# Kernel optimization log

Hardware: AMD Instinct MI355X
Metric: run time of the kernel (lower is better)

Reference implementation:

```python
import jax, jax.numpy as jnp
import numpy as np

EMBED = 1024
HEADS = 16


def setup_inputs() -> dict:
    key = jax.random.key(0)
    ks = jax.random.split(key, 12)
    s = 1.0 / np.sqrt(EMBED)
    return {
        "x": jax.random.normal(ks[0], (1, EMBED, 128, 128), jnp.float32),
        "masks": jax.random.normal(ks[1], (200, 128, 128), jnp.float32),
        "Wq": jax.random.normal(ks[2], (EMBED, EMBED), jnp.float32) * s,
        "bq": jax.random.normal(ks[3], (EMBED,), jnp.float32) * 0.02,
        "Wk": jax.random.normal(ks[4], (EMBED, EMBED), jnp.float32) * s,
        "bk": jax.random.normal(ks[5], (EMBED,), jnp.float32) * 0.02,
        "Wv": jax.random.normal(ks[6], (EMBED, EMBED), jnp.float32) * s,
        "bv": jax.random.normal(ks[7], (EMBED,), jnp.float32) * 0.02,
        "Wc": jax.random.normal(ks[8], (EMBED, EMBED), jnp.float32) * s,
        "bc": jax.random.normal(ks[9], (EMBED,), jnp.float32) * 0.02,
    }


def reference(x, masks, Wq, bq, Wk, bk, Wv, bv, Wc, bc):
    # x: [1, C, H, W], masks: [Q, H, W]  (way4 branch, batch must be 1)
    N, C, H, W = x.shape
    Q = masks.shape[0]
    HW = H * W
    nh = HEADS
    hd = C // nh

    xs = x.reshape(C, HW).T                      # [HW, C] pixel tokens
    m = jax.nn.sigmoid(masks).reshape(Q, HW).T   # [HW, Q]

    # mask-weighted mean pooling (avoid materializing [HW, Q, C])
    w = jnp.sum(m, axis=0)                       # [Q]
    mean = jnp.einsum('lq,lc->qc', m, xs) / (w[:, None] + 0.001)  # [Q, C]

    seq = jnp.concatenate([mean, xs], axis=0)    # [L, C], L = Q + HW
    L = Q + HW

    q = (mean @ Wq.T + bq).reshape(Q, nh, hd) * (hd ** -0.5)
    k = (seq @ Wk.T + bk).reshape(L, nh, hd)
    v = (seq @ Wv.T + bv).reshape(L, nh, hd)

    # bool attn mask [Q, L]: True = disallowed
    qq = ~jnp.eye(Q, dtype=bool)                 # only self among pooled queries
    qp = (m.T <= 0.9)                            # pixels with sigmoid <= 0.9 masked
    attn_mask = jnp.concatenate([qq, qp], axis=1)  # [Q, L]

    scores = jnp.einsum('qhd,lhd->hql', q, k)    # [nh, Q, L]
    scores = jnp.where(attn_mask[None], -jnp.inf, scores)
    probs = jax.nn.softmax(scores, axis=-1)
    ctx = jnp.einsum('hql,lhd->qhd', probs, v).reshape(Q, C)
    out = ctx @ Wc.T + bc                        # [Q, out_dim]
    return out.reshape(Q, 1, -1)                 # match torch [Q, batch=1, out_dim]
```

## Files before the change

### kernel.cpp

```cpp
#include <hip/hip_runtime.h>
#include <math.h>

#define HW_  16384
#define Q_   200
#define C_   1024
#define L_   16584
#define NH_  16
#define HD_  64
#define CAP  512
#define KSPLIT 8
#define KCH  (HW_ / KSPLIT)
#define ASPLIT 4
#define SK   8

typedef __attribute__((ext_vector_type(8))) __bf16 bf16x8;
typedef __attribute__((ext_vector_type(8))) unsigned short u16x8;
typedef __attribute__((ext_vector_type(4))) unsigned short u16x4;
typedef __attribute__((ext_vector_type(4))) float f32x4;

__device__ inline unsigned short f2bf(float f) {
  unsigned int u = __float_as_uint(f);
  u += 0x7fff + ((u >> 16) & 1);
  return (unsigned short)(u >> 16);
}
__device__ inline float bf2f(unsigned short u) {
  return __uint_as_float((unsigned int)u << 16);
}


__global__ __launch_bounds__(256) void k_sig_compact(const float* __restrict__ masks,
                                                     unsigned short* __restrict__ msigbf,
                                                     float* __restrict__ w,
                                                     int* __restrict__ cnt,
                                                     int* __restrict__ idxg) {
  int q = blockIdx.x;
  int tid = threadIdx.x;
  unsigned short* obf = msigbf + (size_t)q * HW_;
  if (q >= Q_) {
    u16x4 z = {0, 0, 0, 0};
    for (int i = tid; i < HW_ / 4; i += 256) *(u16x4*)&obf[i * 4] = z;
    return;
  }
  const float* mrow = masks + (size_t)q * HW_;
  const int base = tid * 64;
  unsigned long long bits = 0;
  float s = 0.f;
  #pragma unroll
  for (int j4 = 0; j4 < 16; j4++) {
    float4 v = *(const float4*)&mrow[base + j4 * 4];
    float sg0 = 1.f / (1.f + expf(-v.x));
    float sg1 = 1.f / (1.f + expf(-v.y));
    float sg2 = 1.f / (1.f + expf(-v.z));
    float sg3 = 1.f / (1.f + expf(-v.w));
    u16x4 o = {f2bf(sg0), f2bf(sg1), f2bf(sg2), f2bf(sg3)};
    *(u16x4*)&obf[base + j4 * 4] = o;
    s += sg0 + sg1 + sg2 + sg3;
    if (sg0 > 0.9f) bits |= 1ull << (j4 * 4 + 0);
    if (sg1 > 0.9f) bits |= 1ull << (j4 * 4 + 1);
    if (sg2 > 0.9f) bits |= 1ull << (j4 * 4 + 2);
    if (sg3 > 0.9f) bits |= 1ull << (j4 * 4 + 3);
  }
  int my = __popcll(bits);

  __shared__ float red[256];
  __shared__ int sc[256];
  red[tid] = s;
  sc[tid] = my;
  __syncthreads();
  for (int off = 128; off > 0; off >>= 1) {
    if (tid < off) red[tid] += red[tid + off];
    __syncthreads();
  }
  if (tid == 0) w[q] = red[0];
  for (int off = 1; off < 256; off <<= 1) {
    int v = sc[tid];
    int add = (tid >= off) ? sc[tid - off] : 0;
    __syncthreads();
    sc[tid] = v + add;
    __syncthreads();
  }
  int excl = sc[tid] - my;
  int total = sc[255];
  int* orow = idxg + (size_t)q * CAP;
  int off = 1 + excl;
  for (int j = 0; j < 64; j++) {
    if ((bits >> j) & 1ull) {
      if (off < CAP) orow[off] = Q_ + base + j;
      off++;
    }
  }
  if (tid == 0) {
    orow[0] = q;
    int c = 1 + total;
    cnt[q] = c < CAP ? c : CAP;
  }
}

__global__ __launch_bounds__(256) void k_xcast(const float* __restrict__ x,
                                               unsigned short* __restrict__ xbf,
                                               unsigned short* __restrict__ seqbf) {
  __shared__ float t[32][33];
  int l0 = blockIdx.x * 32, c0 = blockIdx.y * 32;
  int tx = threadIdx.x, ty = threadIdx.y;
  #pragma unroll
  for (int i = 0; i < 32; i += 8) {
    float v = x[(size_t)(c0 + ty + i) * HW_ + l0 + tx];
    t[ty + i][tx] = v;
    xbf[(size_t)(c0 + ty + i) * HW_ + l0 + tx] = f2bf(v);
  }
  __syncthreads();
  #pragma unroll
  for (int i = 0; i < 32; i += 8)
    seqbf[(size_t)(Q_ + l0 + ty + i) * C_ + c0 + tx] = f2bf(t[tx][ty + i]);
}

__global__ __launch_bounds__(256) void k_cast4(const float* __restrict__ s0,
                                               const float* __restrict__ s1,
                                               const float* __restrict__ s2,
                                               const float* __restrict__ s3,
                                               unsigned short* __restrict__ d0,
                                               unsigned short* __restrict__ d1,
                                               unsigned short* __restrict__ d2,
                                               unsigned short* __restrict__ d3) {
  const float* src = (blockIdx.y == 0) ? s0 : (blockIdx.y == 1) ? s1
                     : (blockIdx.y == 2) ? s2 : s3;
  unsigned short* dst = (blockIdx.y == 0) ? d0 : (blockIdx.y == 1) ? d1
                        : (blockIdx.y == 2) ? d2 : d3;
  int i = (blockIdx.x * 256 + threadIdx.x) * 4;
  float4 v = *(const float4*)&src[i];
  u16x4 o = {f2bf(v.x), f2bf(v.y), f2bf(v.z), f2bf(v.w)};
  *(u16x4*)&dst[i] = o;
}

#define GBM 128
#define GBN 128
#define GBK 32

__global__ __launch_bounds__(256, 2) void k_gemm_kv(const unsigned short* __restrict__ A,
                                                    const unsigned short* __restrict__ Bk,
                                                    const unsigned short* __restrict__ Bv,
                                                    const float* __restrict__ bk,
                                                    const float* __restrict__ bv,
                                                    unsigned short* __restrict__ Ko,
                                                    unsigned short* __restrict__ Vo,
                                                    int M, int K) {
  __shared__ __attribute__((aligned(16))) unsigned short smem[3][3 * GBM * GBK];
  int w = blockIdx.x;
  int nbm = gridDim.x >> 3;
  int t = (w >> 3) + (w & 7) * nbm;
  int bm = (t >> 3) * GBM;
  int bn = (t & 7) * GBN;
  int tid = threadIdx.x;
  int wid = tid >> 6, lane = tid & 63;
  int half = wid >> 1;
  int whalf = wid & 1;
  int fq = lane >> 4, fr = lane & 15;
  int srow = lane >> 2;
  int scol = (((lane & 3) ^ ((lane >> 3) & 3)) * 8);
  int sslot = (fq ^ ((fr >> 1) & 3)) * 8;
  int boff = (half == 0) ? GBM * GBK : 2 * GBM * GBK;

  auto stage = [&](int buf, int k0) {
    #pragma unroll
    for (int i = 0; i < 6; i++) {
      int ci = wid * 6 + i;
      const unsigned short* src;
      if (ci < 8) {
        int gA = bm + ci * 16 + srow; if (gA > M - 1) gA = M - 1;
        src = A + (size_t)gA * K + k0 + scol;
      } else if (ci < 16) {
        src = Bk + (size_t)(bn + (ci - 8) * 16 + srow) * K + k0 + scol;
      } else {
        src = Bv + (size_t)(bn + (ci - 16) * 16 + srow) * K + k0 + scol;
      }
      __builtin_amdgcn_global_load_lds(
          (const __attribute__((address_space(1))) void*)src,
          (__attribute__((address_space(3))) void*)((char*)&smem[buf][0] + ci * 1024),
          16, 0, 0);
    }
  };

  f32x4 acc[4][8] = {};
  const int NT = K / GBK;
  stage(0, 0);
  stage(1, GBK);
  for (int it = 0; it < NT; it++) {
    int cur = it % 3;
    if (it + 2 < NT) {
      stage((it + 2) % 3, (it + 2) * GBK);
      asm volatile("s_waitcnt vmcnt(12)" ::: "memory");
    } else if (it + 1 < NT) {
      asm volatile("s_waitcnt vmcnt(6)" ::: "memory");
    } else {
      asm volatile("s_waitcnt vmcnt(0)" ::: "memory");
    }
    __builtin_amdgcn_s_barrier();
    asm volatile("" ::: "memory");
    const unsigned short (*As)[GBK]  = (const unsigned short (*)[GBK])(&smem[cur][0]);
    const unsigned short (*Bts)[GBK] = (const unsigned short (*)[GBK])(&smem[cur][0] + boff);
    bf16x8 af[4], bfr[8];
    #pragma unroll
    for (int mi = 0; mi < 4; mi++)
      af[mi] = *(const bf16x8*)&As[whalf * 64 + mi * 16 + fr][sslot];
    #pragma unroll
    for (int ni = 0; ni < 8; ni++)
      bfr[ni] = *(const bf16x8*)&Bts[ni * 16 + fr][sslot];
    __builtin_amdgcn_s_setprio(1);
    #pragma unroll
    for (int mi = 0; mi < 4; mi++)
      #pragma unroll
      for (int ni = 0; ni < 8; ni++)
        acc[mi][ni] = __builtin_amdgcn_mfma_f32_16x16x32_bf16(bfr[ni], af[mi], acc[mi][ni], 0, 0, 0);
    __builtin_amdgcn_s_setprio(0);
    asm volatile("" ::: "memory");
    __builtin_amdgcn_s_barrier();
    asm volatile("" ::: "memory");
  }
  const float* bias = (half == 0) ? bk : bv;
  unsigned short* Cout = (half == 0) ? Ko : Vo;
  #pragma unroll
  for (int mi = 0; mi < 4; mi++) {
    int m = bm + whalf * 64 + mi * 16 + fr;
    if (m >= M) continue;
    #pragma unroll
    for (int ni = 0; ni < 8; ni++) {
      int n0 = bn + ni * 16 + fq * 4;
      float4 b4 = *(const float4*)&bias[n0];
      u16x4 o = {f2bf(acc[mi][ni][0] + b4.x), f2bf(acc[mi][ni][1] + b4.y),
                 f2bf(acc[mi][ni][2] + b4.z), f2bf(acc[mi][ni][3] + b4.w)};
      *(u16x4*)&Cout[(size_t)m * C_ + n0] = o;
    }
  }
}

__global__ __launch_bounds__(256) void k_gemm_meank(const unsigned short* __restrict__ A,
                                                    const unsigned short* __restrict__ B,
                                                    float* __restrict__ partial) {
  __shared__ __attribute__((aligned(16))) unsigned short As[2][GBM][GBK];
  __shared__ __attribute__((aligned(16))) unsigned short Bs[2][GBN][GBK];
  int bm = blockIdx.y * GBM, bn = blockIdx.x * GBN;
  int kc = blockIdx.z;
  int tid = threadIdx.x;
  int wid = tid >> 6, lane = tid & 63;
  int wr = wid >> 1, wc = wid & 1;
  int fq = lane >> 4, fr = lane & 15;
  int srow = lane >> 2;
  int scol = (((lane & 3) ^ ((lane >> 3) & 3)) * 8);
  int sslot = (fq ^ ((fr >> 1) & 3)) * 8;

  auto stage = [&](int buf, int k0) {
    #pragma unroll
    for (int i = 0; i < 2; i++) {
      int r = wid * 32 + i * 16 + srow;
      __builtin_amdgcn_global_load_lds(
          (const __attribute__((address_space(1))) void*)(A + (size_t)(bm + r) * HW_ + k0 + scol),
          (__attribute__((address_space(3))) void*)((char*)&As[buf][0][0] + (wid * 2 + i) * 1024),
          16, 0, 0);
      __builtin_amdgcn_global_load_lds(
          (const __attribute__((address_space(1))) void*)(B + (size_t)(bn + r) * HW_ + k0 + scol),
          (__attribute__((address_space(3))) void*)((char*)&Bs[buf][0][0] + (wid * 2 + i) * 1024),
          16, 0, 0);
    }
  };

  f32x4 acc[4][4] = {};
  int kbeg = kc * KCH;
  const int NT = KCH / GBK;
  stage(0, kbeg);
  __syncthreads();
  int cur = 0;
  for (int it = 0; it < NT; it++) {
    if (it + 1 < NT) stage(cur ^ 1, kbeg + (it + 1) * GBK);
    bf16x8 af[4], bfr[4];
    #pragma unroll
    for (int mi = 0; mi < 4; mi++)
      af[mi] = *(const bf16x8*)&As[cur][wr * 64 + mi * 16 + fr][sslot];
    #pragma unroll
    for (int ni = 0; ni < 4; ni++)
      bfr[ni] = *(const bf16x8*)&Bs[cur][wc * 64 + ni * 16 + fr][sslot];
    #pragma unroll
    for (int mi = 0; mi < 4; mi++)
      #pragma unroll
      for (int ni = 0; ni < 4; ni++)
        acc[mi][ni] = __builtin_amdgcn_mfma_f32_16x16x32_bf16(bfr[ni], af[mi], acc[mi][ni], 0, 0, 0);
    __syncthreads();
    cur ^= 1;
  }
  #pragma unroll
  for (int mi = 0; mi < 4; mi++) {
    int m = bm + wr * 64 + mi * 16 + fr;
    #pragma unroll
    for (int ni = 0; ni < 4; ni++) {
      int n0 = bn + wc * 64 + ni * 16 + fq * 4;
      *(f32x4*)&partial[((size_t)kc * 256 + m) * C_ + n0] = acc[mi][ni];
    }
  }
}

__global__ __launch_bounds__(256) void k_mean_reduce(const float* __restrict__ partial,
                                                     const float* __restrict__ w,
                                                     unsigned short* __restrict__ seqbf) {
  int m = blockIdx.x;
  float rs = 1.f / (w[m] + 0.001f);
  for (int n = threadIdx.x; n < C_; n += 256) {
    float s = 0.f;
    #pragma unroll
    for (int kc = 0; kc < KSPLIT; kc++)
      s += partial[((size_t)kc * 256 + m) * C_ + n];
    seqbf[(size_t)m * C_ + n] = f2bf(s * rs);
  }
}

__global__ __launch_bounds__(256) void k_gemm_splitk_bf(const unsigned short* __restrict__ A,
                                                        const unsigned short* __restrict__ B,
                                                        float* __restrict__ partial,
                                                        int M, int K) {
  __shared__ __attribute__((aligned(16))) unsigned short As[2][GBM][GBK];
  __shared__ __attribute__((aligned(16))) unsigned short Bs[2][GBN][GBK];
  int bm = blockIdx.y * GBM, bn = blockIdx.x * GBN;
  int kc = blockIdx.z;
  int kchunk = K / SK;
  int tid = threadIdx.x;
  int wid = tid >> 6, lane = tid & 63;
  int wr = wid >> 1, wc = wid & 1;
  int fq = lane >> 4, fr = lane & 15;
  int srow = lane >> 2;
  int scol = (((lane & 3) ^ ((lane >> 3) & 3)) * 8);
  int sslot = (fq ^ ((fr >> 1) & 3)) * 8;

  auto stage = [&](int buf, int k0) {
    #pragma unroll
    for (int i = 0; i < 2; i++) {
      int r = wid * 32 + i * 16 + srow;
      int gA = bm + r; if (gA > M - 1) gA = M - 1;
      __builtin_amdgcn_global_load_lds(
          (const __attribute__((address_space(1))) void*)(A + (size_t)gA * K + k0 + scol),
          (__attribute__((address_space(3))) void*)((char*)&As[buf][0][0] + (wid * 2 + i) * 1024),
          16, 0, 0);
      __builtin_amdgcn_global_load_lds(
          (const __attribute__((address_space(1))) void*)(B + (size_t)(bn + r) * K + k0 + scol),
          (__attribute__((address_space(3))) void*)((char*)&Bs[buf][0][0] + (wid * 2 + i) * 1024),
          16, 0, 0);
    }
  };

  f32x4 acc[4][4] = {};
  int kbeg = kc * kchunk;
  const int NT = kchunk / GBK;
  stage(0, kbeg);
  __syncthreads();
  int cur = 0;
  for (int it = 0; it < NT; it++) {
    if (it + 1 < NT) stage(cur ^ 1, kbeg + (it + 1) * GBK);
    bf16x8 af[4], bfr[4];
    #pragma unroll
    for (int mi = 0; mi < 4; mi++)
      af[mi] = *(const bf16x8*)&As[cur][wr * 64 + mi * 16 + fr][sslot];
    #pragma unroll
    for (int ni = 0; ni < 4; ni++)
      bfr[ni] = *(const bf16x8*)&Bs[cur][wc * 64 + ni * 16 + fr][sslot];
    #pragma unroll
    for (int mi = 0; mi < 4; mi++)
      #pragma unroll
      for (int ni = 0; ni < 4; ni++)
        acc[mi][ni] = __builtin_amdgcn_mfma_f32_16x16x32_bf16(bfr[ni], af[mi], acc[mi][ni], 0, 0, 0);
    __syncthreads();
    cur ^= 1;
  }
  #pragma unroll
  for (int mi = 0; mi < 4; mi++) {
    int m = bm + wr * 64 + mi * 16 + fr;
    #pragma unroll
    for (int ni = 0; ni < 4; ni++) {
      int n0 = bn + wc * 64 + ni * 16 + fq * 4;
      *(f32x4*)&partial[((size_t)kc * 256 + m) * C_ + n0] = acc[mi][ni];
    }
  }
}

__global__ __launch_bounds__(256) void k_splitk_reduce(const float* __restrict__ partial,
                                                       const float* __restrict__ bias,
                                                       float* __restrict__ outf) {
  int m = blockIdx.x;
  for (int n = threadIdx.x; n < C_; n += 256) {
    float s = 0.f;
    #pragma unroll
    for (int kc = 0; kc < SK; kc++)
      s += partial[((size_t)kc * 256 + m) * C_ + n];
    outf[(size_t)m * C_ + n] = s + bias[n];
  }
}

__global__ __launch_bounds__(256) void k_attn_split(const float* __restrict__ qb,
                                                    const unsigned short* __restrict__ kb,
                                                    const unsigned short* __restrict__ vb,
                                                    const int* __restrict__ cnt_g,
                                                    const int* __restrict__ idxg,
                                                    float* __restrict__ pmax,
                                                    float* __restrict__ psum,
                                                    float* __restrict__ pacc) {
  int q = blockIdx.x, h = blockIdx.y, sp = blockIdx.z;
  int tid = threadIdx.x;
  int lane = tid & 63, wid = tid >> 6;

  __shared__ float qs[64];
  __shared__ float sc[CAP / ASPLIT];
  __shared__ int   ls[CAP / ASPLIT];
  __shared__ float wred[4];
  __shared__ float accb[4][64];

  int cnt = cnt_g[q];
  int cq = (cnt + ASPLIT - 1) / ASPLIT;
  int beg = sp * cq;
  int end = beg + cq; if (end > cnt) end = cnt;
  int ns = end - beg; if (ns < 0) ns = 0;

  if (tid < 64) qs[tid] = qb[(size_t)q * C_ + h * HD_ + tid] * 0.125f;
  __syncthreads();

  if (tid < ns) {
    int l = idxg[(size_t)q * CAP + beg + tid];
    ls[tid] = l;
    const u16x8* kr = (const u16x8*)(kb + (size_t)l * C_ + h * HD_);
    float s = 0.f;
    #pragma unroll
    for (int v8 = 0; v8 < 8; v8++) {
      u16x8 kv = kr[v8];
      #pragma unroll
      for (int e = 0; e < 8; e++) s = fmaf(qs[v8 * 8 + e], bf2f(kv[e]), s);
    }
    sc[tid] = s;
  }
  __syncthreads();

  float lm = (tid < ns) ? sc[tid] : -INFINITY;
  #pragma unroll
  for (int off = 32; off; off >>= 1) lm = fmaxf(lm, __shfl_xor(lm, off));
  if (lane == 0) wred[wid] = lm;
  __syncthreads();
  float m4 = fmaxf(fmaxf(wred[0], wred[1]), fmaxf(wred[2], wred[3]));

  float e = 0.f;
  if (tid < ns) {
    e = expf(sc[tid] - m4);
    sc[tid] = e;
  }
  float lsum = e;
  #pragma unroll
  for (int off = 32; off; off >>= 1) lsum += __shfl_xor(lsum, off);
  __syncthreads();
  if (lane == 0) wred[wid] = lsum;
  __syncthreads();
  float S4 = wred[0] + wred[1] + wred[2] + wred[3];

  float acc = 0.f;
  for (int j = wid; j < ns; j += 4)
    acc = fmaf(sc[j], bf2f(vb[(size_t)ls[j] * C_ + h * HD_ + lane]), acc);
  accb[wid][lane] = acc;
  __syncthreads();

  int pidx = (q * NH_ + h) * ASPLIT + sp;
  if (tid < 64)
    pacc[(size_t)pidx * 64 + tid] =
        accb[0][tid] + accb[1][tid] + accb[2][tid] + accb[3][tid];
  if (tid == 0) {
    pmax[pidx] = (ns > 0) ? m4 : -INFINITY;
    psum[pidx] = S4;
  }
}

__global__ __launch_bounds__(64) void k_attn_merge(const float* __restrict__ pmax,
                                                   const float* __restrict__ psum,
                                                   const float* __restrict__ pacc,
                                                   unsigned short* __restrict__ ctxbf) {
  int q = blockIdx.x, h = blockIdx.y;
  int d = threadIdx.x;
  int base = (q * NH_ + h) * ASPLIT;
  float M = -INFINITY;
  #pragma unroll
  for (int s = 0; s < ASPLIT; s++) M = fmaxf(M, pmax[base + s]);
  float S = 0.f, a = 0.f;
  #pragma unroll
  for (int s = 0; s < ASPLIT; s++) {
    float wgt = expf(pmax[base + s] - M);
    S += psum[base + s] * wgt;
    a += pacc[(size_t)(base + s) * 64 + d] * wgt;
  }
  ctxbf[(size_t)q * C_ + h * HD_ + d] = f2bf(a / S);
}

extern "C" void kernel_launch(void* const* d_in, const int* in_sizes, int n_in,
                              void* d_out, int out_size, void* d_ws, size_t ws_size,
                              hipStream_t stream) {
  const float* x     = (const float*)d_in[0];
  const float* masks = (const float*)d_in[1];
  const float* Wq    = (const float*)d_in[2];
  const float* bq    = (const float*)d_in[3];
  const float* Wk    = (const float*)d_in[4];
  const float* bk    = (const float*)d_in[5];
  const float* Wv    = (const float*)d_in[6];
  const float* bv    = (const float*)d_in[7];
  const float* Wc    = (const float*)d_in[8];
  const float* bc    = (const float*)d_in[9];
  float* out = (float*)d_out;

  char* p = (char*)d_ws;
  auto alloc = [&](size_t bytes) {
    char* r = p;
    p += (bytes + 255) & ~(size_t)255;
    return r;
  };
  float* w       = (float*)alloc(1024);
  float* qbuf    = (float*)alloc((size_t)Q_ * C_ * 4);
  float* partial = (float*)alloc((size_t)KSPLIT * 256 * C_ * 4);
  int*   cnt     = (int*)alloc(1024);
  int*   idxg    = (int*)alloc((size_t)Q_ * CAP * 4);
  float* pmax    = (float*)alloc((size_t)Q_ * NH_ * ASPLIT * 4);
  float* psum    = (float*)alloc((size_t)Q_ * NH_ * ASPLIT * 4);
  float* pacc    = (float*)alloc((size_t)Q_ * NH_ * ASPLIT * 64 * 4);
  unsigned short* msigbf = (unsigned short*)alloc((size_t)256 * HW_ * 2);
  unsigned short* xbf    = (unsigned short*)alloc((size_t)C_ * HW_ * 2);
  unsigned short* seqbf  = (unsigned short*)alloc((size_t)L_ * C_ * 2);
  unsigned short* wkbf   = (unsigned short*)alloc((size_t)C_ * C_ * 2);
  unsigned short* wvbf   = (unsigned short*)alloc((size_t)C_ * C_ * 2);
  unsigned short* wqbf   = (unsigned short*)alloc((size_t)C_ * C_ * 2);
  unsigned short* wcbf   = (unsigned short*)alloc((size_t)C_ * C_ * 2);
  unsigned short* ctxbf  = (unsigned short*)alloc((size_t)256 * C_ * 2);
  unsigned short* kbuf   = (unsigned short*)alloc((size_t)L_ * C_ * 2);
  unsigned short* vbuf   = (unsigned short*)alloc((size_t)L_ * C_ * 2);

  k_sig_compact<<<256, 256, 0, stream>>>(masks, msigbf, w, cnt, idxg);
  k_xcast<<<dim3(HW_ / 32, C_ / 32), dim3(32, 8), 0, stream>>>(x, xbf, seqbf);
  k_cast4<<<dim3(C_ * C_ / 1024, 4), 256, 0, stream>>>(Wk, Wv, Wq, Wc,
                                                       wkbf, wvbf, wqbf, wcbf);
  k_gemm_meank<<<dim3(C_ / GBN, 2, KSPLIT), 256, 0, stream>>>(msigbf, xbf, partial);
  k_mean_reduce<<<Q_, 256, 0, stream>>>(partial, w, seqbf);
  k_gemm_splitk_bf<<<dim3(C_ / GBN, 2, SK), 256, 0, stream>>>(seqbf, wqbf, partial, Q_, C_);
  k_splitk_reduce<<<Q_, 256, 0, stream>>>(partial, bq, qbuf);
  k_gemm_kv<<<8 * ((L_ + GBM - 1) / GBM), 256, 0, stream>>>(
      seqbf, wkbf, wvbf, bk, bv, kbuf, vbuf, L_, C_);
  k_attn_split<<<dim3(Q_, NH_, ASPLIT), 256, 0, stream>>>(
      qbuf, kbuf, vbuf, cnt, idxg, pmax, psum, pacc);
  k_attn_merge<<<dim3(Q_, NH_), 64, 0, stream>>>(pmax, psum, pacc, ctxbf);
  k_gemm_splitk_bf<<<dim3(C_ / GBN, 2, SK), 256, 0, stream>>>(ctxbf, wcbf, partial, Q_, C_);
  k_splitk_reduce<<<Q_, 256, 0, stream>>>(partial, bc, out);
}
```

Measured before the change: 286.2 us.

## Load GEMM B fragments directly to registers and split attention score dot-products

The K/V projection GEMM now loads only the A tile into LDS, with double buffering, and reads B fragments straight from global memory into registers, double-buffered across iterations. This shrinks the shared-memory footprint from a triple-buffered A+Bk+Bv tile to a double-buffered A tile. It drops the occupancy hint, and B loads are no longer shared across waves. The sparse attention score kernel now uses four lanes per key, each handling 16 dims, combined with shuffles, to coalesce loads and spread work. The SK split constant is also reduced from 8 to 4.

```diff
diff --git a/kernel.cpp b/kernel.cpp
--- a/kernel.cpp
+++ b/kernel.cpp
@@ -11,7 +11,7 @@
 #define KSPLIT 8
 #define KCH  (HW_ / KSPLIT)
 #define ASPLIT 4
-#define SK   8
+#define SK   4
 
 typedef __attribute__((ext_vector_type(8))) __bf16 bf16x8;
 typedef __attribute__((ext_vector_type(8))) unsigned short u16x8;
@@ -136,15 +136,15 @@
 #define GBN 128
 #define GBK 32
 
-__global__ __launch_bounds__(256, 2) void k_gemm_kv(const unsigned short* __restrict__ A,
-                                                    const unsigned short* __restrict__ Bk,
-                                                    const unsigned short* __restrict__ Bv,
-                                                    const float* __restrict__ bk,
-                                                    const float* __restrict__ bv,
-                                                    unsigned short* __restrict__ Ko,
-                                                    unsigned short* __restrict__ Vo,
-                                                    int M, int K) {
-  __shared__ __attribute__((aligned(16))) unsigned short smem[3][3 * GBM * GBK];
+__global__ __launch_bounds__(256) void k_gemm_kv(const unsigned short* __restrict__ A,
+                                                 const unsigned short* __restrict__ Bk,
+                                                 const unsigned short* __restrict__ Bv,
+                                                 const float* __restrict__ bk,
+                                                 const float* __restrict__ bv,
+                                                 unsigned short* __restrict__ Ko,
+                                                 unsigned short* __restrict__ Vo,
+                                                 int M, int K) {
+  __shared__ __attribute__((aligned(16))) unsigned short As[2][GBM][GBK];
   int w = blockIdx.x;
   int nbm = gridDim.x >> 3;
   int t = (w >> 3) + (w & 7) * nbm;
@@ -158,53 +158,31 @@
   int srow = lane >> 2;
   int scol = (((lane & 3) ^ ((lane >> 3) & 3)) * 8);
   int sslot = (fq ^ ((fr >> 1) & 3)) * 8;
-  int boff = (half == 0) ? GBM * GBK : 2 * GBM * GBK;
-
-  auto stage = [&](int buf, int k0) {
-    #pragma unroll
-    for (int i = 0; i < 6; i++) {
-      int ci = wid * 6 + i;
-      const unsigned short* src;
-      if (ci < 8) {
-        int gA = bm + ci * 16 + srow; if (gA > M - 1) gA = M - 1;
-        src = A + (size_t)gA * K + k0 + scol;
-      } else if (ci < 16) {
-        src = Bk + (size_t)(bn + (ci - 8) * 16 + srow) * K + k0 + scol;
-      } else {
-        src = Bv + (size_t)(bn + (ci - 16) * 16 + srow) * K + k0 + scol;
-      }
+
+  const unsigned short* Bbase = (half ? Bv : Bk) + (size_t)(bn + fr) * K + fq * 8;
+
+  auto stageA = [&](int buf, int k0) {
+    #pragma unroll
+    for (int i = 0; i < 2; i++) {
+      int ci = wid * 2 + i;
+      int gA = bm + ci * 16 + srow; if (gA > M - 1) gA = M - 1;
       __builtin_amdgcn_global_load_lds(
-          (const __attribute__((address_space(1))) void*)src,
-          (__attribute__((address_space(3))) void*)((char*)&smem[buf][0] + ci * 1024),
+          (const __attribute__((address_space(1))) void*)(A + (size_t)gA * K + k0 + scol),
+          (__attribute__((address_space(3))) void*)((char*)&As[buf][0][0] + ci * 1024),
           16, 0, 0);
     }
   };
-
+  auto loadB = [&](bf16x8 (&bfr)[8], int k0) {
+    #pragma unroll
+    for (int ni = 0; ni < 8; ni++)
+      bfr[ni] = *(const bf16x8*)(Bbase + (size_t)(ni * 16) * K + k0);
+  };
   f32x4 acc[4][8] = {};
-  const int NT = K / GBK;
-  stage(0, 0);
-  stage(1, GBK);
-  for (int it = 0; it < NT; it++) {
-    int cur = it % 3;
-    if (it + 2 < NT) {
-      stage((it + 2) % 3, (it + 2) * GBK);
-      asm volatile("s_waitcnt vmcnt(12)" ::: "memory");
-    } else if (it + 1 < NT) {
-      asm volatile("s_waitcnt vmcnt(6)" ::: "memory");
-    } else {
-      asm volatile("s_waitcnt vmcnt(0)" ::: "memory");
-    }
-    __builtin_amdgcn_s_barrier();
-    asm volatile("" ::: "memory");
-    const unsigned short (*As)[GBK]  = (const unsigned short (*)[GBK])(&smem[cur][0]);
-    const unsigned short (*Bts)[GBK] = (const unsigned short (*)[GBK])(&smem[cur][0] + boff);
-    bf16x8 af[4], bfr[8];
+  auto compute = [&](bf16x8 (&bfr)[8], int buf) {
+    bf16x8 af[4];
     #pragma unroll
     for (int mi = 0; mi < 4; mi++)
-      af[mi] = *(const bf16x8*)&As[whalf * 64 + mi * 16 + fr][sslot];
-    #pragma unroll
-    for (int ni = 0; ni < 8; ni++)
-      bfr[ni] = *(const bf16x8*)&Bts[ni * 16 + fr][sslot];
+      af[mi] = *(const bf16x8*)&As[buf][whalf * 64 + mi * 16 + fr][sslot];
     __builtin_amdgcn_s_setprio(1);
     #pragma unroll
     for (int mi = 0; mi < 4; mi++)
@@ -212,6 +190,26 @@
       for (int ni = 0; ni < 8; ni++)
         acc[mi][ni] = __builtin_amdgcn_mfma_f32_16x16x32_bf16(bfr[ni], af[mi], acc[mi][ni], 0, 0, 0);
     __builtin_amdgcn_s_setprio(0);
+  };
+
+  bf16x8 B0[8], B1[8];
+  const int NT = K / GBK;
+  loadB(B0, 0);
+  stageA(0, 0);
+  for (int it = 0; it < NT; it++) {
+    bool even = !(it & 1);
+    if (it + 1 < NT) {
+      if (even) loadB(B1, (it + 1) * GBK);
+      else      loadB(B0, (it + 1) * GBK);
+      stageA((it + 1) & 1, (it + 1) * GBK);
+      asm volatile("s_waitcnt vmcnt(10)" ::: "memory");
+    } else {
+      asm volatile("s_waitcnt vmcnt(0)" ::: "memory");
+    }
+    __builtin_amdgcn_s_barrier();
+    asm volatile("" ::: "memory");
+    if (even) compute(B0, 0);
+    else      compute(B1, 1);
     asm volatile("" ::: "memory");
     __builtin_amdgcn_s_barrier();
     asm volatile("" ::: "memory");
@@ -418,18 +416,22 @@
   if (tid < 64) qs[tid] = qb[(size_t)q * C_ + h * HD_ + tid] * 0.125f;
   __syncthreads();
 
-  if (tid < ns) {
-    int l = idxg[(size_t)q * CAP + beg + tid];
-    ls[tid] = l;
-    const u16x8* kr = (const u16x8*)(kb + (size_t)l * C_ + h * HD_);
-    float s = 0.f;
-    #pragma unroll
-    for (int v8 = 0; v8 < 8; v8++) {
-      u16x8 kv = kr[v8];
+  for (int i0 = 0; i0 < ns; i0 += 64) {
+    int i = i0 + (tid >> 2);
+    if (i < ns) {
+      int sub = tid & 3;
+      int l = idxg[(size_t)q * CAP + beg + i];
+      const u16x8* kr = (const u16x8*)(kb + (size_t)l * C_ + h * HD_ + sub * 16);
+      u16x8 kv0 = kr[0], kv1 = kr[1];
+      float s = 0.f;
       #pragma unroll
-      for (int e = 0; e < 8; e++) s = fmaf(qs[v8 * 8 + e], bf2f(kv[e]), s);
-    }
-    sc[tid] = s;
+      for (int e = 0; e < 8; e++) s = fmaf(qs[sub * 16 + e], bf2f(kv0[e]), s);
+      #pragma unroll
+      for (int e = 0; e < 8; e++) s = fmaf(qs[sub * 16 + 8 + e], bf2f(kv1[e]), s);
+      s += __shfl_xor(s, 1);
+      s += __shfl_xor(s, 2);
+      if (sub == 0) { sc[i] = s; ls[i] = l; }
+    }
   }
   __syncthreads();
 
```

Result: slower. 550.0 us (+92.1%).

## Use 512-thread KV GEMM blocks, split attention score dot products, halve split-K

Applied to the files above, without the earlier changes.

The fused K/V GEMM now runs 8 waves per block instead of 4. Each wave computes a 64x64 quadrant instead of 64x128, and the staging loads are spread across all waves with adjusted vmcnt waits. The attention score computation now uses 4 lanes per key with shuffle reductions, so more threads take part and each thread issues smaller loads. The split-K factor for the small Q and output projections drops from 8 to 4, which cuts partial-sum traffic but gives those GEMMs less parallelism. The bigger KV block may lower occupancy because the old launch bound asked for 2 blocks per CU.

```diff
diff --git a/kernel.cpp b/kernel.cpp
--- a/kernel.cpp
+++ b/kernel.cpp
@@ -11,7 +11,7 @@
 #define KSPLIT 8
 #define KCH  (HW_ / KSPLIT)
 #define ASPLIT 4
-#define SK   8
+#define SK   4
 
 typedef __attribute__((ext_vector_type(8))) __bf16 bf16x8;
 typedef __attribute__((ext_vector_type(8))) unsigned short u16x8;
@@ -136,14 +136,14 @@
 #define GBN 128
 #define GBK 32
 
-__global__ __launch_bounds__(256, 2) void k_gemm_kv(const unsigned short* __restrict__ A,
-                                                    const unsigned short* __restrict__ Bk,
-                                                    const unsigned short* __restrict__ Bv,
-                                                    const float* __restrict__ bk,
-                                                    const float* __restrict__ bv,
-                                                    unsigned short* __restrict__ Ko,
-                                                    unsigned short* __restrict__ Vo,
-                                                    int M, int K) {
+__global__ __launch_bounds__(512) void k_gemm_kv(const unsigned short* __restrict__ A,
+                                                 const unsigned short* __restrict__ Bk,
+                                                 const unsigned short* __restrict__ Bv,
+                                                 const float* __restrict__ bk,
+                                                 const float* __restrict__ bv,
+                                                 unsigned short* __restrict__ Ko,
+                                                 unsigned short* __restrict__ Vo,
+                                                 int M, int K) {
   __shared__ __attribute__((aligned(16))) unsigned short smem[3][3 * GBM * GBK];
   int w = blockIdx.x;
   int nbm = gridDim.x >> 3;
@@ -152,18 +152,18 @@
   int bn = (t & 7) * GBN;
   int tid = threadIdx.x;
   int wid = tid >> 6, lane = tid & 63;
-  int half = wid >> 1;
-  int whalf = wid & 1;
+  int w2 = wid & 3;
+  int wr = w2 >> 1, wc = w2 & 1;
   int fq = lane >> 4, fr = lane & 15;
   int srow = lane >> 2;
   int scol = (((lane & 3) ^ ((lane >> 3) & 3)) * 8);
   int sslot = (fq ^ ((fr >> 1) & 3)) * 8;
-  int boff = (half == 0) ? GBM * GBK : 2 * GBM * GBK;
+  int boff = (wid < 4) ? GBM * GBK : 2 * GBM * GBK;
 
   auto stage = [&](int buf, int k0) {
     #pragma unroll
-    for (int i = 0; i < 6; i++) {
-      int ci = wid * 6 + i;
+    for (int i = 0; i < 3; i++) {
+      int ci = wid * 3 + i;
       const unsigned short* src;
       if (ci < 8) {
         int gA = bm + ci * 16 + srow; if (gA > M - 1) gA = M - 1;
@@ -180,7 +180,7 @@
     }
   };
 
-  f32x4 acc[4][8] = {};
+  f32x4 acc[4][4] = {};
   const int NT = K / GBK;
   stage(0, 0);
   stage(1, GBK);
@@ -188,9 +188,9 @@
     int cur = it % 3;
     if (it + 2 < NT) {
       stage((it + 2) % 3, (it + 2) * GBK);
-      asm volatile("s_waitcnt vmcnt(12)" ::: "memory");
+      asm volatile("s_waitcnt vmcnt(6)" ::: "memory");
     } else if (it + 1 < NT) {
-      asm volatile("s_waitcnt vmcnt(6)" ::: "memory");
+      asm volatile("s_waitcnt vmcnt(3)" ::: "memory");
     } else {
       asm volatile("s_waitcnt vmcnt(0)" ::: "memory");
     }
@@ -198,33 +198,33 @@
     asm volatile("" ::: "memory");
     const unsigned short (*As)[GBK]  = (const unsigned short (*)[GBK])(&smem[cur][0]);
     const unsigned short (*Bts)[GBK] = (const unsigned short (*)[GBK])(&smem[cur][0] + boff);
-    bf16x8 af[4], bfr[8];
+    bf16x8 af[4], bfr[4];
     #pragma unroll
     for (int mi = 0; mi < 4; mi++)
-      af[mi] = *(const bf16x8*)&As[whalf * 64 + mi * 16 + fr][sslot];
-    #pragma unroll
-    for (int ni = 0; ni < 8; ni++)
-      bfr[ni] = *(const bf16x8*)&Bts[ni * 16 + fr][sslot];
+      af[mi] = *(const bf16x8*)&As[wr * 64 + mi * 16 + fr][sslot];
+    #pragma unroll
+    for (int ni = 0; ni < 4; ni++)
+      bfr[ni] = *(const bf16x8*)&Bts[wc * 64 + ni * 16 + fr][sslot];
     __builtin_amdgcn_s_setprio(1);
     #pragma unroll
     for (int mi = 0; mi < 4; mi++)
       #pragma unroll
-      for (int ni = 0; ni < 8; ni++)
+      for (int ni = 0; ni < 4; ni++)
         acc[mi][ni] = __builtin_amdgcn_mfma_f32_16x16x32_bf16(bfr[ni], af[mi], acc[mi][ni], 0, 0, 0);
     __builtin_amdgcn_s_setprio(0);
     asm volatile("" ::: "memory");
     __builtin_amdgcn_s_barrier();
     asm volatile("" ::: "memory");
   }
-  const float* bias = (half == 0) ? bk : bv;
-  unsigned short* Cout = (half == 0) ? Ko : Vo;
+  const float* bias = (wid < 4) ? bk : bv;
+  unsigned short* Cout = (wid < 4) ? Ko : Vo;
   #pragma unroll
   for (int mi = 0; mi < 4; mi++) {
-    int m = bm + whalf * 64 + mi * 16 + fr;
+    int m = bm + wr * 64 + mi * 16 + fr;
     if (m >= M) continue;
     #pragma unroll
-    for (int ni = 0; ni < 8; ni++) {
-      int n0 = bn + ni * 16 + fq * 4;
+    for (int ni = 0; ni < 4; ni++) {
+      int n0 = bn + wc * 64 + ni * 16 + fq * 4;
       float4 b4 = *(const float4*)&bias[n0];
       u16x4 o = {f2bf(acc[mi][ni][0] + b4.x), f2bf(acc[mi][ni][1] + b4.y),
                  f2bf(acc[mi][ni][2] + b4.z), f2bf(acc[mi][ni][3] + b4.w)};
@@ -418,18 +418,22 @@
   if (tid < 64) qs[tid] = qb[(size_t)q * C_ + h * HD_ + tid] * 0.125f;
   __syncthreads();
 
-  if (tid < ns) {
-    int l = idxg[(size_t)q * CAP + beg + tid];
-    ls[tid] = l;
-    const u16x8* kr = (const u16x8*)(kb + (size_t)l * C_ + h * HD_);
-    float s = 0.f;
-    #pragma unroll
-    for (int v8 = 0; v8 < 8; v8++) {
-      u16x8 kv = kr[v8];
+  for (int i0 = 0; i0 < ns; i0 += 64) {
+    int i = i0 + (tid >> 2);
+    if (i < ns) {
+      int sub = tid & 3;
+      int l = idxg[(size_t)q * CAP + beg + i];
+      const u16x8* kr = (const u16x8*)(kb + (size_t)l * C_ + h * HD_ + sub * 16);
+      u16x8 kv0 = kr[0], kv1 = kr[1];
+      float s = 0.f;
       #pragma unroll
-      for (int e = 0; e < 8; e++) s = fmaf(qs[v8 * 8 + e], bf2f(kv[e]), s);
-    }
-    sc[tid] = s;
+      for (int e = 0; e < 8; e++) s = fmaf(qs[sub * 16 + e], bf2f(kv0[e]), s);
+      #pragma unroll
+      for (int e = 0; e < 8; e++) s = fmaf(qs[sub * 16 + 8 + e], bf2f(kv1[e]), s);
+      s += __shfl_xor(s, 1);
+      s += __shfl_xor(s, 2);
+      if (sub == 0) { sc[i] = s; ls[i] = l; }
+    }
   }
   __syncthreads();
 
@@ -537,7 +541,7 @@
   k_mean_reduce<<<Q_, 256, 0, stream>>>(partial, w, seqbf);
   k_gemm_splitk_bf<<<dim3(C_ / GBN, 2, SK), 256, 0, stream>>>(seqbf, wqbf, partial, Q_, C_);
   k_splitk_reduce<<<Q_, 256, 0, stream>>>(partial, bq, qbuf);
-  k_gemm_kv<<<8 * ((L_ + GBM - 1) / GBM), 256, 0, stream>>>(
+  k_gemm_kv<<<8 * ((L_ + GBM - 1) / GBM), 512, 0, stream>>>(
       seqbf, wkbf, wvbf, bk, bv, kbuf, vbuf, L_, C_);
   k_attn_split<<<dim3(Q_, NH_, ASPLIT), 256, 0, stream>>>(
       qbuf, kbuf, vbuf, cnt, idxg, pmax, psum, pacc);
```

After: 272.4 us. -4.8%, faster.
